# Optimization experiments

Measured on AMD Instinct MI355X. Metric: run time of the kernel, lower is better.

The kernel has to match this reference:

```python
import jax, jax.numpy as jnp
import numpy as np

MAXV = 127.0  # 2**(8-1) - 1, signed int8


def setup_inputs() -> dict:
    key = jax.random.key(0)
    k1, k2, k3 = jax.random.split(key, 3)
    N, K, M = 8192, 4096, 4096  # tokens, size_in, size_out
    x = jax.random.normal(k1, (N, K), dtype=jnp.float32)
    weight = jax.random.normal(k2, (M, K), dtype=jnp.float32) * 0.02
    bias = jax.random.normal(k3, (M,), dtype=jnp.float32) * 0.01
    amax_x = jnp.array([3.0], dtype=jnp.float32)   # calibrated activation amax
    amax_w = jnp.array([0.06], dtype=jnp.float32)  # calibrated weight amax
    return {"x": x, "weight": weight, "bias": bias, "amax_x": amax_x, "amax_w": amax_w}


def _quantize_int8(v, amax):
    # TensorQuantizer with fake_quant=False: scale to int grid, round, clamp to [-127, 127]
    return jnp.clip(jnp.round(v * (MAXV / amax)), -MAXV, MAXV).astype(jnp.int8)


def reference(x, weight, bias, amax_x, amax_w):
    qx = _quantize_int8(x, amax_x)          # [N, K] int8
    qw = _quantize_int8(weight, amax_w)     # [M, K] int8
    acc = jnp.matmul(qx.astype(jnp.int32), qw.T.astype(jnp.int32))  # [N, M] int32
    scale = (MAXV / amax_x) * (MAXV / amax_w)  # combined dequant scale
    out = acc.astype(jnp.float32) / scale
    return out + bias
```

## Files before the change

kernel.cpp:

```cpp
#include <hip/hip_runtime.h>

typedef __attribute__((ext_vector_type(4))) int i32x4;

__device__ __forceinline__ void gload_lds16(const void* g, void* l) {
  __builtin_amdgcn_global_load_lds((const __attribute__((address_space(1))) void*)g,
                                   (__attribute__((address_space(3))) void*)l,
                                   16, 0, 0);
}

#define BARRIER() __builtin_amdgcn_s_barrier()
#define LGKM0()   asm volatile("s_waitcnt lgkmcnt(0)" ::: "memory")
#define VMCNT3()  asm volatile("s_waitcnt vmcnt(3)" ::: "memory")

__global__ void quant_both_kernel(const float* __restrict__ x,
                                  const float* __restrict__ w,
                                  signed char* __restrict__ qx,
                                  signed char* __restrict__ qw,
                                  const float* __restrict__ amax_x,
                                  const float* __restrict__ amax_w,
                                  int nx4, int nw4) {
  const float sx = 127.0f / amax_x[0];
  const float sw = 127.0f / amax_w[0];
  int i = blockIdx.x * blockDim.x + threadIdx.x;
  const int stride = gridDim.x * blockDim.x;
  const int ntot = nx4 + nw4;
  for (; i < ntot; i += stride) {
    const bool isx = i < nx4;
    const float4* src = isx ? (const float4*)x : (const float4*)w;
    int* dst = isx ? (int*)qx : (int*)qw;
    const int j = isx ? i : i - nx4;
    const float s = isx ? sx : sw;
    float4 v = src[j];
    int q0 = (int)rintf(fminf(fmaxf(v.x * s, -127.0f), 127.0f));
    int q1 = (int)rintf(fminf(fmaxf(v.y * s, -127.0f), 127.0f));
    int q2 = (int)rintf(fminf(fmaxf(v.z * s, -127.0f), 127.0f));
    int q3 = (int)rintf(fminf(fmaxf(v.w * s, -127.0f), 127.0f));
    dst[j] = (q0 & 255) | ((q1 & 255) << 8) | ((q2 & 255) << 16) | ((q3 & 255) << 24);
  }
}

__global__ __launch_bounds__(512, 4) void gemm_i8_bk64(
    const signed char* __restrict__ qx,
    const signed char* __restrict__ qw,
    const float* __restrict__ bias,
    const float* __restrict__ amax_x,
    const float* __restrict__ amax_w,
    float* __restrict__ out,
    int N, int M, int K) {
  constexpr int BKB = 64;

  __shared__ signed char lds[49152];

  const int tid  = threadIdx.x;
  const int lane = tid & 63;
  const int wid  = tid >> 6;
  const int wm   = wid >> 2;
  const int wn   = wid & 3;
  const int l15  = lane & 15;
  const int l4   = lane >> 4;

  const int nbn = M >> 7;
  const int nwg = (N >> 8) * nbn;
  const int cpx = nwg >> 3;
  const int swz = (blockIdx.x & 7) * cpx + (blockIdx.x >> 3);
  const int rowBase = (swz / nbn) << 8;
  const int colBase = (swz % nbn) << 7;

  const signed char* srcA[2];
#pragma unroll
  for (int L = 0; L < 2; ++L) {
    const int slot = L * 512 + tid;
    const int row  = slot >> 2;
    const int c    = (slot & 3) ^ ((row >> 1) & 3);
    srcA[L] = qx + (size_t)(rowBase + row) * K + c * 16;
  }
  const int rowB = tid >> 2;
  const int cB   = (tid & 3) ^ ((rowB >> 1) & 3);
  const signed char* srcB = qw + (size_t)(colBase + rowB) * K + cB * 16;

  signed char* A[2] = {lds, lds + 16384};
  signed char* B[2] = {lds + 32768, lds + 40960};

#define STAGE(p, kt)                                                   \
  do {                                                                 \
    gload_lds16(srcA[0] + (kt) * BKB, A[p] + tid * 16);                \
    gload_lds16(srcA[1] + (kt) * BKB, A[p] + 8192 + tid * 16);         \
    gload_lds16(srcB + (kt) * BKB, B[p] + tid * 16);                   \
  } while (0)

  i32x4 acc[8][2] = {{{0}}};
  i32x4 af[8];
  i32x4 bf[2];

  int offA[8], offB[2];
#pragma unroll
  for (int mi = 0; mi < 8; ++mi) {
    const int r = wm * 128 + mi * 16 + l15;
    offA[mi] = r * 64 + ((l4 ^ ((r >> 1) & 3)) * 16);
  }
#pragma unroll
  for (int nj = 0; nj < 2; ++nj) {
    const int r = wn * 32 + nj * 16 + l15;
    offB[nj] = r * 64 + ((l4 ^ ((r >> 1) & 3)) * 16);
  }

#define PHASE(p, ktStage)                                                     \
  do {                                                                        \
    _Pragma("unroll") for (int mi = 0; mi < 8; ++mi)                          \
        af[mi] = *(const i32x4*)(A[p] + offA[mi]);                            \
    _Pragma("unroll") for (int nj = 0; nj < 2; ++nj)                          \
        bf[nj] = *(const i32x4*)(B[p] + offB[nj]);                            \
    LGKM0();                                                                  \
    BARRIER();                          \
    STAGE(p, ktStage);                                                        \
    __builtin_amdgcn_s_setprio(1);                                            \
    _Pragma("unroll") for (int mi = 0; mi < 8; ++mi)                          \
        _Pragma("unroll") for (int nj = 0; nj < 2; ++nj)                      \
            acc[mi][nj] = __builtin_amdgcn_mfma_i32_16x16x64_i8(              \
                af[mi], bf[nj], acc[mi][nj], 0, 0, 0);                        \
    __builtin_amdgcn_s_setprio(0);                                            \
    VMCNT3();             \
    BARRIER();                                          \
  } while (0)

  const int T = K / BKB;

  STAGE(0, 0);
  STAGE(1, 1);
  VMCNT3();
  BARRIER();

  for (int it = 0; it < T / 2; ++it) {
    const int k2 = (2 * it + 2 < T) ? 2 * it + 2 : T - 1;
    const int k3 = (2 * it + 3 < T) ? 2 * it + 3 : T - 1;
    PHASE(0, k2);
    PHASE(1, k3);
  }

  const float dq = amax_x[0] * amax_w[0] * (1.0f / (127.0f * 127.0f));
#pragma unroll
  for (int nj = 0; nj < 2; ++nj) {
    const int col = colBase + wn * 32 + nj * 16 + l15;
    const float bv = bias[col];
#pragma unroll
    for (int mi = 0; mi < 8; ++mi) {
      const int row = rowBase + wm * 128 + mi * 16 + l4 * 4;
#pragma unroll
      for (int r = 0; r < 4; ++r)
        out[(size_t)(row + r) * M + col] = (float)acc[mi][nj][r] * dq + bv;
    }
  }
#undef STAGE
#undef PHASE
}

extern "C" void kernel_launch(void* const* d_in, const int* in_sizes, int n_in,
                              void* d_out, int out_size, void* d_ws, size_t ws_size,
                              hipStream_t stream) {
  const float* x      = (const float*)d_in[0];
  const float* w      = (const float*)d_in[1];
  const float* bias   = (const float*)d_in[2];
  const float* amax_x = (const float*)d_in[3];
  const float* amax_w = (const float*)d_in[4];
  float* out = (float*)d_out;

  const int M = in_sizes[2];
  const int K = in_sizes[1] / M;
  const int N = (int)((long)in_sizes[0] / K);

  signed char* qx = (signed char*)d_ws;
  signed char* qw = qx + (size_t)N * K;

  const int nx4 = N * (K / 4);
  const int nw4 = M * (K / 4);
  quant_both_kernel<<<2048, 256, 0, stream>>>(x, w, qx, qw, amax_x, amax_w,
                                              nx4, nw4);

  const int nwg = (N / 256) * (M / 128);
  gemm_i8_bk64<<<nwg, 512, 0, stream>>>(qx, qw, bias, amax_x, amax_w, out,
                                        N, M, K);
}
```

Measured before the change: 217.4 us.

## Switch GEMM to 256x256 tiles with 32x32x32 int8 MFMA and BK=128

Replaces the 256x128 tile / BK=64 int8 GEMM with a 256x256 tile, a K-step of 128 bytes and the 32x32x32 int8 MFMA, using a 128 KB double-buffered LDS with a new XOR swizzle. Each K-step is split into four sub-phases that read LDS fragments while the next tile's global->LDS loads are issued. The larger tile is meant to raise arithmetic intensity and cut global/LDS traffic per MFMA. In exchange it lowers occupancy (launch bounds 2, large LDS), halves the workgroup count, and adds more barriers per K-step.

```diff
diff --git a/kernel.cpp b/kernel.cpp
--- a/kernel.cpp
+++ b/kernel.cpp
@@ -1,6 +1,7 @@
 #include <hip/hip_runtime.h>
 
 typedef __attribute__((ext_vector_type(4))) int i32x4;
+typedef __attribute__((ext_vector_type(16))) int i32x16;
 
 __device__ __forceinline__ void gload_lds16(const void* g, void* l) {
   __builtin_amdgcn_global_load_lds((const __attribute__((address_space(1))) void*)g,
@@ -10,7 +11,7 @@
 
 #define BARRIER() __builtin_amdgcn_s_barrier()
 #define LGKM0()   asm volatile("s_waitcnt lgkmcnt(0)" ::: "memory")
-#define VMCNT3()  asm volatile("s_waitcnt vmcnt(3)" ::: "memory")
+#define VMCNT0()  asm volatile("s_waitcnt vmcnt(0)" ::: "memory")
 
 __global__ void quant_both_kernel(const float* __restrict__ x,
                                   const float* __restrict__ w,
@@ -39,7 +40,7 @@
   }
 }
 
-__global__ __launch_bounds__(512, 4) void gemm_i8_bk64(
+__global__ __launch_bounds__(512, 2) void gemm_i8_ks(
     const signed char* __restrict__ qx,
     const signed char* __restrict__ qw,
     const float* __restrict__ bias,
@@ -47,111 +48,140 @@
     const float* __restrict__ amax_w,
     float* __restrict__ out,
     int N, int M, int K) {
-  constexpr int BKB = 64;
-
-  __shared__ signed char lds[49152];
+  constexpr int BKB = 128;
+
+  __shared__ signed char lds[4][256 * 128];
 
   const int tid  = threadIdx.x;
   const int lane = tid & 63;
   const int wid  = tid >> 6;
   const int wm   = wid >> 2;
   const int wn   = wid & 3;
-  const int l15  = lane & 15;
-  const int l4   = lane >> 4;
-
-  const int nbn = M >> 7;
+  const int l31  = lane & 31;
+  const int l1   = lane >> 5;
+
+  const int nbn = M >> 8;
   const int nwg = (N >> 8) * nbn;
   const int cpx = nwg >> 3;
   const int swz = (blockIdx.x & 7) * cpx + (blockIdx.x >> 3);
   const int rowBase = (swz / nbn) << 8;
-  const int colBase = (swz % nbn) << 7;
-
-  const signed char* srcA[2];
-#pragma unroll
-  for (int L = 0; L < 2; ++L) {
-    const int slot = L * 512 + tid;
-    const int row  = slot >> 2;
-    const int c    = (slot & 3) ^ ((row >> 1) & 3);
-    srcA[L] = qx + (size_t)(rowBase + row) * K + c * 16;
-  }
-  const int rowB = tid >> 2;
-  const int cB   = (tid & 3) ^ ((rowB >> 1) & 3);
-  const signed char* srcB = qw + (size_t)(colBase + rowB) * K + cB * 16;
-
-  signed char* A[2] = {lds, lds + 16384};
-  signed char* B[2] = {lds + 32768, lds + 40960};
-
-#define STAGE(p, kt)                                                   \
-  do {                                                                 \
-    gload_lds16(srcA[0] + (kt) * BKB, A[p] + tid * 16);                \
-    gload_lds16(srcA[1] + (kt) * BKB, A[p] + 8192 + tid * 16);         \
-    gload_lds16(srcB + (kt) * BKB, B[p] + tid * 16);                   \
+  const int colBase = (swz % nbn) << 8;
+
+  const signed char* sA[2][2];
+  const signed char* sB[2][2];
+#pragma unroll
+  for (int h = 0; h < 2; ++h)
+#pragma unroll
+    for (int L = 0; L < 2; ++L) {
+      const int slot = h * 1024 + L * 512 + tid;
+      const int row  = slot >> 3;
+      const int c    = (slot & 7) ^ (row & 7);
+      sA[h][L] = qx + (size_t)(rowBase + row) * K + c * 16;
+      sB[h][L] = qw + (size_t)(colBase + row) * K + c * 16;
+    }
+
+  signed char* A0 = lds[0];
+  signed char* B0 = lds[1];
+  signed char* A1 = lds[2];
+  signed char* B1 = lds[3];
+
+#define STAGE(dst, src, h, kt)                                                \
+  do {                                                                        \
+    gload_lds16(src[h][0] + (kt) * BKB, (dst) + (h)*16384 + tid * 16);        \
+    gload_lds16(src[h][1] + (kt) * BKB, (dst) + (h)*16384 + 8192 + tid * 16); \
   } while (0)
 
-  i32x4 acc[8][2] = {{{0}}};
-  i32x4 af[8];
+  int ck[4];
+#pragma unroll
+  for (int q = 0; q < 4; ++q) ck[q] = ((2 * q + l1) ^ (l31 & 7)) * 16;
+  const int aBase = (wm * 128 + l31) * 128;
+  const int bBase = (wn * 64 + l31) * 128;
+
+  i32x16 acc[4][2] = {{{0}}};
+  i32x4 af[4];
   i32x4 bf[2];
 
-  int offA[8], offB[2];
-#pragma unroll
-  for (int mi = 0; mi < 8; ++mi) {
-    const int r = wm * 128 + mi * 16 + l15;
-    offA[mi] = r * 64 + ((l4 ^ ((r >> 1) & 3)) * 16);
-  }
-#pragma unroll
-  for (int nj = 0; nj < 2; ++nj) {
-    const int r = wn * 32 + nj * 16 + l15;
-    offB[nj] = r * 64 + ((l4 ^ ((r >> 1) & 3)) * 16);
-  }
-
-#define PHASE(p, ktStage)                                                     \
-  do {                                                                        \
-    _Pragma("unroll") for (int mi = 0; mi < 8; ++mi)                          \
-        af[mi] = *(const i32x4*)(A[p] + offA[mi]);                            \
+#define RDQ(RA, RB, q)                                                        \
+  {                                                                           \
+    _Pragma("unroll") for (int mi = 0; mi < 4; ++mi)                          \
+        af[mi] = *(const i32x4*)((RA) + aBase + mi * 4096 + ck[q]);           \
     _Pragma("unroll") for (int nj = 0; nj < 2; ++nj)                          \
-        bf[nj] = *(const i32x4*)(B[p] + offB[nj]);                            \
-    LGKM0();                                                                  \
-    BARRIER();                          \
-    STAGE(p, ktStage);                                                        \
+        bf[nj] = *(const i32x4*)((RB) + bBase + nj * 4096 + ck[q]);           \
+  }
+#define MFMA8()                                                               \
+  {                                                                           \
     __builtin_amdgcn_s_setprio(1);                                            \
-    _Pragma("unroll") for (int mi = 0; mi < 8; ++mi)                          \
+    _Pragma("unroll") for (int mi = 0; mi < 4; ++mi)                          \
         _Pragma("unroll") for (int nj = 0; nj < 2; ++nj)                      \
-            acc[mi][nj] = __builtin_amdgcn_mfma_i32_16x16x64_i8(              \
+            acc[mi][nj] = __builtin_amdgcn_mfma_i32_32x32x32_i8(              \
                 af[mi], bf[nj], acc[mi][nj], 0, 0, 0);                        \
     __builtin_amdgcn_s_setprio(0);                                            \
-    VMCNT3();             \
-    BARRIER();                                          \
-  } while (0)
+  }
 
   const int T = K / BKB;
 
-  STAGE(0, 0);
-  STAGE(1, 1);
-  VMCNT3();
+  STAGE(A0, sA, 0, 0); STAGE(A0, sA, 1, 0);
+  STAGE(B0, sB, 0, 0); STAGE(B0, sB, 1, 0);
+  VMCNT0();
   BARRIER();
 
   for (int it = 0; it < T / 2; ++it) {
+    const int k1 = 2 * it + 1;
     const int k2 = (2 * it + 2 < T) ? 2 * it + 2 : T - 1;
-    const int k3 = (2 * it + 3 < T) ? 2 * it + 3 : T - 1;
-    PHASE(0, k2);
-    PHASE(1, k3);
-  }
+
+    RDQ(A0, B0, 0);
+    STAGE(A1, sA, 0, k1); STAGE(B1, sB, 0, k1);
+    BARRIER(); LGKM0(); MFMA8(); BARRIER();
+
+    RDQ(A0, B0, 1);
+    STAGE(A1, sA, 1, k1); STAGE(B1, sB, 1, k1);
+    BARRIER(); LGKM0(); MFMA8(); BARRIER();
+
+    RDQ(A0, B0, 2);
+    BARRIER(); LGKM0(); MFMA8(); BARRIER();
+
+    RDQ(A0, B0, 3);
+    BARRIER(); LGKM0(); MFMA8();
+    VMCNT0();
+    BARRIER();
+
+    RDQ(A1, B1, 0);
+    STAGE(A0, sA, 0, k2); STAGE(B0, sB, 0, k2);
+    BARRIER(); LGKM0(); MFMA8(); BARRIER();
+
+    RDQ(A1, B1, 1);
+    STAGE(A0, sA, 1, k2); STAGE(B0, sB, 1, k2);
+    BARRIER(); LGKM0(); MFMA8(); BARRIER();
+
+    RDQ(A1, B1, 2);
+    BARRIER(); LGKM0(); MFMA8(); BARRIER();
+
+    RDQ(A1, B1, 3);
+    BARRIER(); LGKM0(); MFMA8();
+    VMCNT0();
+    BARRIER();
+  }
+
+  VMCNT0();
 
   const float dq = amax_x[0] * amax_w[0] * (1.0f / (127.0f * 127.0f));
 #pragma unroll
   for (int nj = 0; nj < 2; ++nj) {
-    const int col = colBase + wn * 32 + nj * 16 + l15;
+    const int col = colBase + wn * 64 + nj * 32 + l31;
     const float bv = bias[col];
 #pragma unroll
-    for (int mi = 0; mi < 8; ++mi) {
-      const int row = rowBase + wm * 128 + mi * 16 + l4 * 4;
-#pragma unroll
-      for (int r = 0; r < 4; ++r)
-        out[(size_t)(row + r) * M + col] = (float)acc[mi][nj][r] * dq + bv;
+    for (int mi = 0; mi < 4; ++mi) {
+      const int rowF = rowBase + wm * 128 + mi * 32 + 4 * l1;
+#pragma unroll
+      for (int r = 0; r < 16; ++r) {
+        const int row = rowF + (r & 3) + 8 * (r >> 2);
+        out[(size_t)row * M + col] = (float)acc[mi][nj][r] * dq + bv;
+      }
     }
   }
 #undef STAGE
-#undef PHASE
+#undef RDQ
+#undef MFMA8
 }
 
 extern "C" void kernel_launch(void* const* d_in, const int* in_sizes, int n_in,
@@ -176,7 +206,7 @@
   quant_both_kernel<<<2048, 256, 0, stream>>>(x, w, qx, qw, amax_x, amax_w,
                                               nx4, nw4);
 
-  const int nwg = (N / 256) * (M / 128);
-  gemm_i8_bk64<<<nwg, 512, 0, stream>>>(qx, qw, bias, amax_x, amax_w, out,
-                                        N, M, K);
-}
+  const int nwg = (N / 256) * (M / 256);
+  gemm_i8_ks<<<nwg, 512, 0, stream>>>(qx, qw, bias, amax_x, amax_w, out,
+                                      N, M, K);
+}
```

New measurement: 199.4 us. -8.3%, faster.

## Enlarge GEMM tile to 256x256, load B directly to registers, BK=128

Applied to the files above, without the earlier changes.

The int8 GEMM tile grows from 256x128 to 256x256 and BK from 64 to 128. B fragments are now loaded straight from global memory into double-buffered registers instead of being staged through LDS, so LDS holds only double-buffered A tiles with a new XOR swizzle. Each wave's accumulator footprint doubles and launch bounds drop to 2 blocks per CU. The aim is more arithmetic per byte loaded and less LDS traffic, at the cost of higher register pressure, lower occupancy, and uncoalesced direct B global loads.

```diff
diff --git a/kernel.cpp b/kernel.cpp
--- a/kernel.cpp
+++ b/kernel.cpp
@@ -9,8 +9,7 @@
 }
 
 #define BARRIER() __builtin_amdgcn_s_barrier()
-#define LGKM0()   asm volatile("s_waitcnt lgkmcnt(0)" ::: "memory")
-#define VMCNT3()  asm volatile("s_waitcnt vmcnt(3)" ::: "memory")
+#define VMCNT0()  asm volatile("s_waitcnt vmcnt(0)" ::: "memory")
 
 __global__ void quant_both_kernel(const float* __restrict__ x,
                                   const float* __restrict__ w,
@@ -39,7 +38,7 @@
   }
 }
 
-__global__ __launch_bounds__(512, 4) void gemm_i8_bk64(
+__global__ __launch_bounds__(512, 2) void gemm_i8_bdir(
     const signed char* __restrict__ qx,
     const signed char* __restrict__ qw,
     const float* __restrict__ bias,
@@ -47,9 +46,9 @@
     const float* __restrict__ amax_w,
     float* __restrict__ out,
     int N, int M, int K) {
-  constexpr int BKB = 64;
+  constexpr int BKB = 128;
 
-  __shared__ signed char lds[49152];
+  __shared__ signed char Ald[2][256 * 128];
 
   const int tid  = threadIdx.x;
   const int lane = tid & 63;
@@ -59,88 +58,96 @@
   const int l15  = lane & 15;
   const int l4   = lane >> 4;
 
-  const int nbn = M >> 7;
+  const int nbn = M >> 8;
   const int nwg = (N >> 8) * nbn;
   const int cpx = nwg >> 3;
   const int swz = (blockIdx.x & 7) * cpx + (blockIdx.x >> 3);
   const int rowBase = (swz / nbn) << 8;
-  const int colBase = (swz % nbn) << 7;
+  const int colBase = (swz % nbn) << 8;
 
-  const signed char* srcA[2];
+  const signed char* sA[2][2];
 #pragma unroll
-  for (int L = 0; L < 2; ++L) {
-    const int slot = L * 512 + tid;
-    const int row  = slot >> 2;
-    const int c    = (slot & 3) ^ ((row >> 1) & 3);
-    srcA[L] = qx + (size_t)(rowBase + row) * K + c * 16;
-  }
-  const int rowB = tid >> 2;
-  const int cB   = (tid & 3) ^ ((rowB >> 1) & 3);
-  const signed char* srcB = qw + (size_t)(colBase + rowB) * K + cB * 16;
+  for (int h = 0; h < 2; ++h)
+#pragma unroll
+    for (int L = 0; L < 2; ++L) {
+      const int slot = h * 1024 + L * 512 + tid;
+      const int row  = slot >> 3;
+      const int c    = (slot & 7) ^ (row & 7);
+      sA[h][L] = qx + (size_t)(rowBase + row) * K + c * 16;
+    }
 
-  signed char* A[2] = {lds, lds + 16384};
-  signed char* B[2] = {lds + 32768, lds + 40960};
+  const signed char* sB[4];
+#pragma unroll
+  for (int nj = 0; nj < 4; ++nj)
+    sB[nj] = qw + (size_t)(colBase + wn * 64 + nj * 16 + l15) * K + l4 * 16;
 
-#define STAGE(p, kt)                                                   \
-  do {                                                                 \
-    gload_lds16(srcA[0] + (kt) * BKB, A[p] + tid * 16);                \
-    gload_lds16(srcA[1] + (kt) * BKB, A[p] + 8192 + tid * 16);         \
-    gload_lds16(srcB + (kt) * BKB, B[p] + tid * 16);                   \
+#define STAGEA(p, kt)                                                    \
+  do {                                                                   \
+    gload_lds16(sA[0][0] + (kt) * BKB, Ald[p] + tid * 16);               \
+    gload_lds16(sA[0][1] + (kt) * BKB, Ald[p] + 8192 + tid * 16);        \
+    gload_lds16(sA[1][0] + (kt) * BKB, Ald[p] + 16384 + tid * 16);       \
+    gload_lds16(sA[1][1] + (kt) * BKB, Ald[p] + 24576 + tid * 16);       \
   } while (0)
 
-  i32x4 acc[8][2] = {{{0}}};
-  i32x4 af[8];
-  i32x4 bf[2];
+  const int ck0 = ((l4) ^ (l15 & 7)) * 16;
+  const int ck1 = ((4 + l4) ^ (l15 & 7)) * 16;
+  const int aBase = (wm * 128 + l15) * 128;
 
-  int offA[8], offB[2];
-#pragma unroll
-  for (int mi = 0; mi < 8; ++mi) {
-    const int r = wm * 128 + mi * 16 + l15;
-    offA[mi] = r * 64 + ((l4 ^ ((r >> 1) & 3)) * 16);
-  }
-#pragma unroll
-  for (int nj = 0; nj < 2; ++nj) {
-    const int r = wn * 32 + nj * 16 + l15;
-    offB[nj] = r * 64 + ((l4 ^ ((r >> 1) & 3)) * 16);
+  i32x4 acc[8][4] = {{{0}}};
+  i32x4 bregE[4][2], bregO[4][2];
+
+#define LOADB(DST, kt)                                                   \
+  {                                                                      \
+    _Pragma("unroll") for (int nj = 0; nj < 4; ++nj) {                   \
+      DST[nj][0] = *(const i32x4*)(sB[nj] + (kt) * BKB);                 \
+      DST[nj][1] = *(const i32x4*)(sB[nj] + (kt) * BKB + 64);            \
+    }                                                                    \
   }
 
-#define PHASE(p, ktStage)                                                     \
-  do {                                                                        \
-    _Pragma("unroll") for (int mi = 0; mi < 8; ++mi)                          \
-        af[mi] = *(const i32x4*)(A[p] + offA[mi]);                            \
-    _Pragma("unroll") for (int nj = 0; nj < 2; ++nj)                          \
-        bf[nj] = *(const i32x4*)(B[p] + offB[nj]);                            \
-    LGKM0();                                                                  \
-    BARRIER();                          \
-    STAGE(p, ktStage);                                                        \
-    __builtin_amdgcn_s_setprio(1);                                            \
-    _Pragma("unroll") for (int mi = 0; mi < 8; ++mi)                          \
-        _Pragma("unroll") for (int nj = 0; nj < 2; ++nj)                      \
-            acc[mi][nj] = __builtin_amdgcn_mfma_i32_16x16x64_i8(              \
-                af[mi], bf[nj], acc[mi][nj], 0, 0, 0);                        \
-    __builtin_amdgcn_s_setprio(0);                                            \
-    VMCNT3();             \
-    BARRIER();                                          \
-  } while (0)
+#define QPHASE(p, mh, ks, BREG)                                          \
+  {                                                                      \
+    i32x4 af[4];                                                         \
+    _Pragma("unroll") for (int q = 0; q < 4; ++q)                        \
+        af[q] = *(const i32x4*)(Ald[p] + aBase + (mh) * 8192 + q * 2048  \
+                                + ((ks) ? ck1 : ck0));                   \
+    __builtin_amdgcn_s_setprio(1);                                       \
+    _Pragma("unroll") for (int q = 0; q < 4; ++q)                        \
+        _Pragma("unroll") for (int nj = 0; nj < 4; ++nj)                 \
+            acc[(mh) * 4 + q][nj] = __builtin_amdgcn_mfma_i32_16x16x64_i8( \
+                af[q], BREG[nj][ks], acc[(mh) * 4 + q][nj], 0, 0, 0);    \
+    __builtin_amdgcn_s_setprio(0);                                       \
+  }
+
+#define KTILE(p, BCUR, BNXT, ktNext)                                     \
+  {                                                                      \
+    LOADB(BNXT, ktNext);                                                 \
+    STAGEA(p ^ 1, ktNext);                                               \
+    QPHASE(p, 0, 0, BCUR);                                               \
+    QPHASE(p, 0, 1, BCUR);                                               \
+    QPHASE(p, 1, 0, BCUR);                                               \
+    QPHASE(p, 1, 1, BCUR);                                               \
+    VMCNT0();           \
+    BARRIER();                                                           \
+  }
 
   const int T = K / BKB;
 
-  STAGE(0, 0);
-  STAGE(1, 1);
-  VMCNT3();
+  LOADB(bregE, 0);
+  STAGEA(0, 0);
+  VMCNT0();
   BARRIER();
 
   for (int it = 0; it < T / 2; ++it) {
-    const int k2 = (2 * it + 2 < T) ? 2 * it + 2 : T - 1;
-    const int k3 = (2 * it + 3 < T) ? 2 * it + 3 : T - 1;
-    PHASE(0, k2);
-    PHASE(1, k3);
+    const int t1 = 2 * it + 1;
+    const int t2 = (2 * it + 2 < T) ? 2 * it + 2 : T - 1;
+    KTILE(0, bregE, bregO, t1);
+    KTILE(1, bregO, bregE, t2);
   }
 
   const float dq = amax_x[0] * amax_w[0] * (1.0f / (127.0f * 127.0f));
 #pragma unroll
-  for (int nj = 0; nj < 2; ++nj) {
-    const int col = colBase + wn * 32 + nj * 16 + l15;
+  for (int nj = 0; nj < 4; ++nj) {
+    const int col = colBase + wn * 64 + nj * 16 + l15;
     const float bv = bias[col];
 #pragma unroll
     for (int mi = 0; mi < 8; ++mi) {
@@ -150,8 +157,10 @@
         out[(size_t)(row + r) * M + col] = (float)acc[mi][nj][r] * dq + bv;
     }
   }
-#undef STAGE
-#undef PHASE
+#undef STAGEA
+#undef LOADB
+#undef QPHASE
+#undef KTILE
 }
 
 extern "C" void kernel_launch(void* const* d_in, const int* in_sizes, int n_in,
@@ -176,7 +185,7 @@
   quant_both_kernel<<<2048, 256, 0, stream>>>(x, w, qx, qw, amax_x, amax_w,
                                               nx4, nw4);
 
-  const int nwg = (N / 256) * (M / 128);
-  gemm_i8_bk64<<<nwg, 512, 0, stream>>>(qx, qw, bias, amax_x, amax_w, out,
+  const int nwg = (N / 256) * (M / 256);
+  gemm_i8_bdir<<<nwg, 512, 0, stream>>>(qx, qw, bias, amax_x, amax_w, out,
                                         N, M, K);
 }
```

After: 257.3 us. 1.18x slower.
